# Optimization experiments

Hardware: AMD Instinct MI355X
Metric: run time of the kernel (lower is better)

## Reference

```python
import jax, jax.numpy as jnp
import numpy as np

N = 50000
E = 1600000
F_IN = 4
F_OUT = 32
PERIODS = 12


def setup_inputs() -> dict:
    key = jax.random.key(0)
    ks = jax.random.split(key, 18)
    s_in = 1.0 / np.sqrt(F_IN)
    s_cat = 1.0 / np.sqrt(2 * F_OUT)
    s_out = 1.0 / np.sqrt(F_OUT)
    inp = {
        'x': jax.random.normal(ks[0], (N, F_IN, PERIODS), dtype=jnp.float32),
        'edge_index': jax.random.randint(ks[1], (2, E), 0, N, dtype=jnp.int32),
        'attention': jax.random.uniform(ks[2], (PERIODS,), dtype=jnp.float32),
        # GRU update gate z: GCNConv weight/bias + Linear(2*F_OUT -> F_OUT)
        'Wz': jax.random.normal(ks[3], (F_IN, F_OUT), jnp.float32) * s_in,
        'bz': jnp.zeros((F_OUT,), jnp.float32),
        'Lz': jax.random.normal(ks[4], (2 * F_OUT, F_OUT), jnp.float32) * s_cat,
        'lz': jnp.zeros((F_OUT,), jnp.float32),
        # reset gate r
        'Wr': jax.random.normal(ks[5], (F_IN, F_OUT), jnp.float32) * s_in,
        'br': jnp.zeros((F_OUT,), jnp.float32),
        'Lr': jax.random.normal(ks[6], (2 * F_OUT, F_OUT), jnp.float32) * s_cat,
        'lr': jnp.zeros((F_OUT,), jnp.float32),
        # candidate h
        'Wh': jax.random.normal(ks[7], (F_IN, F_OUT), jnp.float32) * s_in,
        'bh': jnp.zeros((F_OUT,), jnp.float32),
        'Lh': jax.random.normal(ks[8], (2 * F_OUT, F_OUT), jnp.float32) * s_cat,
        'lh': jnp.zeros((F_OUT,), jnp.float32),
        # outer Linear(32 -> periods)
        'Wo': jax.random.normal(ks[9], (F_OUT, PERIODS), jnp.float32) * s_out,
        'bo': jnp.zeros((PERIODS,), jnp.float32),
    }
    return inp


def reference(x, edge_index, attention, Wz, bz, Lz, lz, Wr, br, Lr, lr, Wh, bh, Lh, lh, Wo, bo):
    n = x.shape[0]
    # gcn_norm: add self loops, symmetric D^-1/2 (A+I) D^-1/2
    loop = jnp.arange(n, dtype=edge_index.dtype)
    row = jnp.concatenate([edge_index[0], loop])  # source
    col = jnp.concatenate([edge_index[1], loop])  # target
    w = jnp.ones(row.shape[0], dtype=x.dtype)
    deg = jax.ops.segment_sum(w, col, num_segments=n)
    dinv = jnp.where(deg > 0, jax.lax.rsqrt(deg), 0.0)
    norm = dinv[row] * dinv[col]  # [E+N]

    def conv(xt, W, b):
        h = xt @ W                                   # [N, F_OUT]
        msg = h[row] * norm[:, None]                 # gather + scale
        return jax.ops.segment_sum(msg, col, num_segments=n) + b

    H0 = jnp.zeros((n, F_OUT), dtype=x.dtype)  # A3TGCN passes H=None each period

    def tgcn(xt):
        Z = jax.nn.sigmoid(jnp.concatenate([conv(xt, Wz, bz), H0], axis=1) @ Lz + lz)
        R = jax.nn.sigmoid(jnp.concatenate([conv(xt, Wr, br), H0], axis=1) @ Lr + lr)
        Ht = jnp.tanh(jnp.concatenate([conv(xt, Wh, bh), H0 * R], axis=1) @ Lh + lh)
        return Z * H0 + (1.0 - Z) * Ht

    Hs = jax.vmap(tgcn)(jnp.moveaxis(x, 2, 0))       # [T, N, F_OUT]
    probs = jax.nn.softmax(attention)
    H = jnp.einsum('tnc,t->nc', Hs, probs)           # attention-weighted sum over periods
    return jax.nn.relu(H) @ Wo + bo                  # [N, PERIODS]
```

## Files before the change

kernel.cpp:

```cpp
#include <hip/hip_runtime.h>
#include <hip/hip_fp16.h>
#include <math.h>

#define CHUNK 6144
#define CAPG  10240
#define GNODES 42

union U4H { uint4 u; __half2 h[4]; };

__global__ void k_pre(const float* __restrict__ Wz, const float* __restrict__ Lz, const float* __restrict__ lz,
                      const float* __restrict__ Wh, const float* __restrict__ Lh, const float* __restrict__ lh,
                      const float* __restrict__ bz, const float* __restrict__ bh,
                      const float* __restrict__ att,
                      float* __restrict__ AzT, float* __restrict__ AhT,
                      float* __restrict__ bzp, float* __restrict__ bhp, float* __restrict__ probs,
                      int* __restrict__ gcur) {
  int t = threadIdx.x;
  gcur[t] = 0;
  if (t < 128) {
    int f = t >> 2, k = t & 3;
    float s = 0.f, s2 = 0.f;
    for (int j = 0; j < 32; ++j) {
      s  = fmaf(Wz[k * 32 + j], Lz[j * 32 + f], s);
      s2 = fmaf(Wh[k * 32 + j], Lh[j * 32 + f], s2);
    }
    AzT[t] = s; AhT[t] = s2;
  }
  if (t >= 128 && t < 160) {
    int f = t - 128;
    float s = lz[f], s2 = lh[f];
    for (int j = 0; j < 32; ++j) {
      s  = fmaf(bz[j], Lz[j * 32 + f], s);
      s2 = fmaf(bh[j], Lh[j * 32 + f], s2);
    }
    bzp[f] = s; bhp[f] = s2;
  }
  if (t == 160) {
    float m = att[0];
    for (int i = 1; i < 12; ++i) m = fmaxf(m, att[i]);
    float e[12]; float s = 0.f;
    for (int i = 0; i < 12; ++i) { e[i] = __expf(att[i] - m); s += e[i]; }
    for (int i = 0; i < 12; ++i) probs[i] = e[i] / s;
  }
}

__global__ __launch_bounds__(1024) void k_part(const int* __restrict__ row, const int* __restrict__ col,
                                               int E, int nbkt,
                                               int* __restrict__ gcur, unsigned* __restrict__ part) {
  __shared__ unsigned spak[CHUNK];
  __shared__ unsigned char sbkt[CHUNK];
  __shared__ unsigned char slc[CHUNK];
  __shared__ int hist[256], sscan[256], scur[256], gbase[256];
  int t = threadIdx.x;
  int base = blockIdx.x * CHUNK;
  int cnt = E - base; if (cnt > CHUNK) cnt = CHUNK;
  if (t < 256) hist[t] = 0;
  __syncthreads();
  for (int i = t; i < cnt; i += 1024) {
    int c = col[base + i];
    int b = c >> 8;
    sbkt[i] = (unsigned char)b;
    slc[i]  = (unsigned char)(c & 255);
    atomicAdd(&hist[b], 1);
  }
  __syncthreads();
  int v = 0;
  if (t < 256) { v = hist[t]; sscan[t] = v; }
  __syncthreads();
  for (int off = 1; off < 256; off <<= 1) {
    int a = 0;
    if (t < 256 && t >= off) a = sscan[t - off];
    __syncthreads();
    if (t < 256) sscan[t] += a;
    __syncthreads();
  }
  if (t < 256) {
    sscan[t] -= v;
    gbase[t] = (v > 0) ? atomicAdd(&gcur[t], v) : 0;
    scur[t] = 0;
  }
  __syncthreads();
  for (int i = t; i < cnt; i += 1024) {
    int r = row[base + i];
    int b = sbkt[i];
    int pos = atomicAdd(&scur[b], 1);
    spak[sscan[b] + pos] = ((unsigned)r << 8) | (unsigned)slc[i];
  }
  __syncthreads();
  int wave = t >> 6, lane = t & 63;
  for (int b = wave; b < nbkt; b += 16) {
    int len = hist[b], gb = gbase[b], src = sscan[b];
    int lim = CAPG - gb; if (lim > len) lim = len;
    unsigned* dst = part + (size_t)b * CAPG + gb;
    for (int j = lane; j < lim; j += 64) dst[j] = spak[src + j];
  }
}

__global__ __launch_bounds__(1024) void k_sort(const unsigned* __restrict__ part, const int* __restrict__ gcur,
                                               const float4* __restrict__ x4,
                                               int* __restrict__ csr, int2* __restrict__ rng,
                                               float* __restrict__ dinv, uint2* __restrict__ xh2, int n) {
  __shared__ int hist[256], soff[256], scur2[256];
  __shared__ float sdi[256];
  int b = blockIdx.x, t = threadIdx.x;
  int cnt = gcur[b]; if (cnt > CAPG) cnt = CAPG;
  const unsigned* src = part + (size_t)b * CAPG;
  if (t < 256) hist[t] = 0;
  __syncthreads();
  for (int i = t; i < cnt; i += 1024) atomicAdd(&hist[src[i] & 255u], 1);
  __syncthreads();
  int v = 0;
  if (t < 256) { v = hist[t]; soff[t] = v; }
  __syncthreads();
  for (int off = 1; off < 256; off <<= 1) {
    int a = 0;
    if (t < 256 && t >= off) a = soff[t - off];
    __syncthreads();
    if (t < 256) soff[t] += a;
    __syncthreads();
  }
  int base = b * CAPG;
  if (t < 256) {
    int excl = soff[t] - v;
    int node = b * 256 + t;
    float di = rsqrtf((float)(v + 1));
    sdi[t] = di;
    if (node < n) {
      rng[node] = make_int2(base + excl, base + excl + v);
      dinv[node] = di;
    }
    soff[t] = excl;
    scur2[t] = 0;
  }
  __syncthreads();
  for (int i = t; i < cnt; i += 1024) {
    unsigned e = src[i];
    int lc = (int)(e & 255u);
    int pos = atomicAdd(&scur2[lc], 1);
    csr[base + soff[lc] + pos] = (int)(e >> 8);
  }
  int gb = b * 3072;
  for (int j = t; j < 3072; j += 1024) {
    int gi = gb + j;
    if (gi < n * 12) {
      float4 f = x4[gi];
      float d = sdi[j / 12];
      __half2 h0 = __floats2half2_rn(d * f.x, d * f.y);
      __half2 h1 = __floats2half2_rn(d * f.z, d * f.w);
      uint2 u; u.x = *(unsigned*)&h0; u.y = *(unsigned*)&h1;
      xh2[gi] = u;
    }
  }
}

__global__ __launch_bounds__(256) void k_gather(const int* __restrict__ csr, const int2* __restrict__ rng,
                                                const float* __restrict__ dinv, const uint4* __restrict__ xh4,
                                                const float* __restrict__ AzT, const float* __restrict__ AhT,
                                                const float* __restrict__ bzp, const float* __restrict__ bhp,
                                                const float* __restrict__ probs,
                                                const float* __restrict__ Wo, const float* __restrict__ bo,
                                                float* __restrict__ out, int n) {
  __shared__ float sY[GNODES * 49];
  __shared__ float4 sAz4[32], sAh4[32];
  __shared__ float sbzp[32], sbhp[32], sprobs[12], sbo[12], sWo[384];
  int t = threadIdx.x;
  int nb = blockIdx.x * GNODES;

  if (t < 32) {
    sAz4[t] = ((const float4*)AzT)[t];
    sAh4[t] = ((const float4*)AhT)[t];
    sbzp[t] = bzp[t]; sbhp[t] = bhp[t];
  }
  if (t >= 32 && t < 44) { sprobs[t - 32] = probs[t - 32]; sbo[t - 32] = bo[t - 32]; }
  for (int i = t; i < 384; i += 256) sWo[i] = Wo[i];

  int grp = t / 6, c = t - grp * 6;
  int node = nb + grp;
  if (t < GNODES * 6 && node < n) {
    U4H u; u.u = xh4[(size_t)node * 6 + c];
    float2 f0 = __half22float2(u.h[0]), f1 = __half22float2(u.h[1]);
    float2 f2 = __half22float2(u.h[2]), f3 = __half22float2(u.h[3]);
    float a0 = f0.x, a1 = f0.y, a2 = f1.x, a3 = f1.y;
    float a4 = f2.x, a5 = f2.y, a6 = f3.x, a7 = f3.y;
    int2 r = rng[node];
    int e = r.x, end = r.y;
    for (; e + 4 <= end; e += 4) {
      int r0 = csr[e], r1 = csr[e + 1], r2 = csr[e + 2], r3 = csr[e + 3];
      U4H v0, v1, v2, v3;
      v0.u = xh4[(size_t)r0 * 6 + c];
      v1.u = xh4[(size_t)r1 * 6 + c];
      v2.u = xh4[(size_t)r2 * 6 + c];
      v3.u = xh4[(size_t)r3 * 6 + c];
#define ACC8(V) { \
      float2 g0 = __half22float2(V.h[0]), g1 = __half22float2(V.h[1]); \
      float2 g2 = __half22float2(V.h[2]), g3 = __half22float2(V.h[3]); \
      a0 += g0.x; a1 += g0.y; a2 += g1.x; a3 += g1.y; \
      a4 += g2.x; a5 += g2.y; a6 += g3.x; a7 += g3.y; }
      ACC8(v0) ACC8(v1) ACC8(v2) ACC8(v3)
    }
    for (; e < end; ++e) {
      int r0 = csr[e];
      U4H v0; v0.u = xh4[(size_t)r0 * 6 + c];
      ACC8(v0)
    }
#undef ACC8
    float di = dinv[node];
    float* yb = sY + grp * 49 + c * 8;
    yb[0] = a0 * di; yb[1] = a1 * di; yb[2] = a2 * di; yb[3] = a3 * di;
    yb[4] = a4 * di; yb[5] = a5 * di; yb[6] = a6 * di; yb[7] = a7 * di;
  }
  __syncthreads();

  if (t < GNODES) {
    int node2 = nb + t;
    if (node2 < n) {
      const float* y = sY + t * 49;
      float H[32];
      for (int f = 0; f < 32; ++f) {
        float4 az = sAz4[f], ah = sAh4[f];
        float bzf = sbzp[f], bhf = sbhp[f];
        float acc = 0.f;
#pragma unroll
        for (int tt = 0; tt < 12; ++tt) {
          float y0 = y[tt], y1 = y[12 + tt], y2 = y[24 + tt], y3 = y[36 + tt];
          float za = fmaf(az.x, y0, fmaf(az.y, y1, fmaf(az.z, y2, fmaf(az.w, y3, bzf))));
          float ha = fmaf(ah.x, y0, fmaf(ah.y, y1, fmaf(ah.z, y2, fmaf(ah.w, y3, bhf))));
          float ez = __expf(za);
          float ax = fabsf(ha);
          float e2 = __expf(-2.f * ax);
          float g = (1.f - e2) / ((1.f + ez) * (1.f + e2));
          acc = fmaf(sprobs[tt], copysignf(g, ha), acc);
        }
        H[f] = fmaxf(acc, 0.f);
      }
#pragma unroll
      for (int p = 0; p < 12; ++p) {
        float acc = sbo[p];
#pragma unroll
        for (int f = 0; f < 32; ++f) acc = fmaf(H[f], sWo[f * 12 + p], acc);
        out[node2 * 12 + p] = acc;
      }
    }
  }
}

extern "C" void kernel_launch(void* const* d_in, const int* in_sizes, int n_in,
                              void* d_out, int out_size, void* d_ws, size_t ws_size,
                              hipStream_t stream) {
  const float* x   = (const float*)d_in[0];
  const int*   ei  = (const int*)d_in[1];
  const float* att = (const float*)d_in[2];
  const float* Wz  = (const float*)d_in[3];
  const float* bz  = (const float*)d_in[4];
  const float* Lz  = (const float*)d_in[5];
  const float* lz  = (const float*)d_in[6];
  const float* Wh  = (const float*)d_in[11];
  const float* bh  = (const float*)d_in[12];
  const float* Lh  = (const float*)d_in[13];
  const float* lh  = (const float*)d_in[14];
  const float* Wo  = (const float*)d_in[15];
  const float* bo  = (const float*)d_in[16];
  float* out = (float*)d_out;

  const int N = in_sizes[0] / (4 * 12);
  const int E = in_sizes[1] / 2;
  const int NBKT = (N + 255) >> 8;
  const int* row = ei;
  const int* col = ei + E;

  char* w = (char*)d_ws;
  size_t o = 0;
  auto alloc = [&](size_t bytes) -> char* {
    o = (o + 255) & ~(size_t)255;
    char* p = w + o; o += bytes; return p;
  };
  float* pAzT   = (float*)alloc(128 * 4);
  float* pAhT   = (float*)alloc(128 * 4);
  float* pbzp   = (float*)alloc(32 * 4);
  float* pbhp   = (float*)alloc(32 * 4);
  float* pprobs = (float*)alloc(12 * 4);
  int*   pgcur  = (int*)alloc(256 * 4);
  float* pdinv  = (float*)alloc((size_t)NBKT * 256 * 4);
  int2*  prng   = (int2*)alloc((size_t)N * 8);
  unsigned* ppart = (unsigned*)alloc((size_t)256 * CAPG * 4);
  int*   pcsr   = (int*)alloc((size_t)256 * CAPG * 4);
  uint2* pxh    = (uint2*)alloc((size_t)NBKT * 256 * 12 * 8);
  (void)ws_size; (void)n_in; (void)out_size;

  k_pre<<<1, 256, 0, stream>>>(Wz, Lz, lz, Wh, Lh, lh, bz, bh, att,
                               pAzT, pAhT, pbzp, pbhp, pprobs, pgcur);
  k_part<<<(E + CHUNK - 1) / CHUNK, 1024, 0, stream>>>(row, col, E, NBKT, pgcur, ppart);
  k_sort<<<NBKT, 1024, 0, stream>>>(ppart, pgcur, (const float4*)x, pcsr, prng, pdinv, pxh, N);
  k_gather<<<(N + GNODES - 1) / GNODES, 256, 0, stream>>>(pcsr, prng, pdinv, (const uint4*)pxh,
                                                          pAzT, pAhT, pbzp, pbhp, pprobs,
                                                          Wo, bo, out, N);
}
```

Measured before the change: 207.6 us.

## Split gather and dense stages into separate kernels with finer thread mapping

```diff
diff --git a/kernel.cpp b/kernel.cpp
--- a/kernel.cpp
+++ b/kernel.cpp
@@ -4,9 +4,9 @@
 
 #define CHUNK 6144
 #define CAPG  10240
-#define GNODES 42
-
-union U4H { uint4 u; __half2 h[4]; };
+#define GNODES 21
+
+union U2H { uint2 u; __half2 h[2]; };
 
 __global__ void k_pre(const float* __restrict__ Wz, const float* __restrict__ Lz, const float* __restrict__ lz,
                       const float* __restrict__ Wh, const float* __restrict__ Lh, const float* __restrict__ lh,
@@ -154,92 +154,104 @@
 }
 
 __global__ __launch_bounds__(256) void k_gather(const int* __restrict__ csr, const int2* __restrict__ rng,
-                                                const float* __restrict__ dinv, const uint4* __restrict__ xh4,
-                                                const float* __restrict__ AzT, const float* __restrict__ AhT,
-                                                const float* __restrict__ bzp, const float* __restrict__ bhp,
-                                                const float* __restrict__ probs,
-                                                const float* __restrict__ Wo, const float* __restrict__ bo,
-                                                float* __restrict__ out, int n) {
-  __shared__ float sY[GNODES * 49];
+                                                const float* __restrict__ dinv, const uint2* __restrict__ xh2,
+                                                float4* __restrict__ Y4, int n) {
+  int t = threadIdx.x;
+  int grp = t / 12, c = t - grp * 12;
+  if (grp >= GNODES) return;
+  int node = blockIdx.x * GNODES + grp;
+  if (node >= n) return;
+  U2H s; s.u = xh2[(size_t)node * 12 + c];
+  float2 f0 = __half22float2(s.h[0]), f1 = __half22float2(s.h[1]);
+  float a0 = f0.x, a1 = f0.y, a2 = f1.x, a3 = f1.y;
+  int2 r = rng[node];
+  int e = r.x, end = r.y;
+#define ACC4(V) { \
+    float2 g0 = __half22float2(V.h[0]), g1 = __half22float2(V.h[1]); \
+    a0 += g0.x; a1 += g0.y; a2 += g1.x; a3 += g1.y; }
+  for (; e + 8 <= end; e += 8) {
+    int r0 = csr[e],     r1 = csr[e + 1], r2 = csr[e + 2], r3 = csr[e + 3];
+    int r4 = csr[e + 4], r5 = csr[e + 5], r6 = csr[e + 6], r7 = csr[e + 7];
+    U2H v0, v1, v2, v3, v4, v5, v6, v7;
+    v0.u = xh2[(size_t)r0 * 12 + c];
+    v1.u = xh2[(size_t)r1 * 12 + c];
+    v2.u = xh2[(size_t)r2 * 12 + c];
+    v3.u = xh2[(size_t)r3 * 12 + c];
+    v4.u = xh2[(size_t)r4 * 12 + c];
+    v5.u = xh2[(size_t)r5 * 12 + c];
+    v6.u = xh2[(size_t)r6 * 12 + c];
+    v7.u = xh2[(size_t)r7 * 12 + c];
+    ACC4(v0) ACC4(v1) ACC4(v2) ACC4(v3) ACC4(v4) ACC4(v5) ACC4(v6) ACC4(v7)
+  }
+  for (; e < end; ++e) {
+    int r0 = csr[e];
+    U2H v0; v0.u = xh2[(size_t)r0 * 12 + c];
+    ACC4(v0)
+  }
+#undef ACC4
+  float di = dinv[node];
+  Y4[(size_t)node * 12 + c] = make_float4(a0 * di, a1 * di, a2 * di, a3 * di);
+}
+
+__global__ __launch_bounds__(256) void k_dense(
+    const float4* __restrict__ Y4,
+    const float* __restrict__ AzT, const float* __restrict__ AhT,
+    const float* __restrict__ bzp, const float* __restrict__ bhp,
+    const float* __restrict__ probs,
+    const float* __restrict__ Wo, const float* __restrict__ bo,
+    float* __restrict__ out, int n) {
   __shared__ float4 sAz4[32], sAh4[32];
-  __shared__ float sbzp[32], sbhp[32], sprobs[12], sbo[12], sWo[384];
+  __shared__ float sbzp[32], sbhp[32], sprobs[12], sbo[12];
+  __shared__ float sWo[384];
+  __shared__ float4 sY4[96];
+  __shared__ float sH[8 * 33];
+
   int t = threadIdx.x;
-  int nb = blockIdx.x * GNODES;
+  int nb = blockIdx.x * 8;
 
   if (t < 32) {
     sAz4[t] = ((const float4*)AzT)[t];
     sAh4[t] = ((const float4*)AhT)[t];
-    sbzp[t] = bzp[t]; sbhp[t] = bhp[t];
+    sbzp[t] = bzp[t];
+    sbhp[t] = bhp[t];
   }
   if (t >= 32 && t < 44) { sprobs[t - 32] = probs[t - 32]; sbo[t - 32] = bo[t - 32]; }
   for (int i = t; i < 384; i += 256) sWo[i] = Wo[i];
-
-  int grp = t / 6, c = t - grp * 6;
-  int node = nb + grp;
-  if (t < GNODES * 6 && node < n) {
-    U4H u; u.u = xh4[(size_t)node * 6 + c];
-    float2 f0 = __half22float2(u.h[0]), f1 = __half22float2(u.h[1]);
-    float2 f2 = __half22float2(u.h[2]), f3 = __half22float2(u.h[3]);
-    float a0 = f0.x, a1 = f0.y, a2 = f1.x, a3 = f1.y;
-    float a4 = f2.x, a5 = f2.y, a6 = f3.x, a7 = f3.y;
-    int2 r = rng[node];
-    int e = r.x, end = r.y;
-    for (; e + 4 <= end; e += 4) {
-      int r0 = csr[e], r1 = csr[e + 1], r2 = csr[e + 2], r3 = csr[e + 3];
-      U4H v0, v1, v2, v3;
-      v0.u = xh4[(size_t)r0 * 6 + c];
-      v1.u = xh4[(size_t)r1 * 6 + c];
-      v2.u = xh4[(size_t)r2 * 6 + c];
-      v3.u = xh4[(size_t)r3 * 6 + c];
-#define ACC8(V) { \
-      float2 g0 = __half22float2(V.h[0]), g1 = __half22float2(V.h[1]); \
-      float2 g2 = __half22float2(V.h[2]), g3 = __half22float2(V.h[3]); \
-      a0 += g0.x; a1 += g0.y; a2 += g1.x; a3 += g1.y; \
-      a4 += g2.x; a5 += g2.y; a6 += g3.x; a7 += g3.y; }
-      ACC8(v0) ACC8(v1) ACC8(v2) ACC8(v3)
-    }
-    for (; e < end; ++e) {
-      int r0 = csr[e];
-      U4H v0; v0.u = xh4[(size_t)r0 * 6 + c];
-      ACC8(v0)
-    }
-#undef ACC8
-    float di = dinv[node];
-    float* yb = sY + grp * 49 + c * 8;
-    yb[0] = a0 * di; yb[1] = a1 * di; yb[2] = a2 * di; yb[3] = a3 * di;
-    yb[4] = a4 * di; yb[5] = a5 * di; yb[6] = a6 * di; yb[7] = a7 * di;
-  }
-  __syncthreads();
-
-  if (t < GNODES) {
-    int node2 = nb + t;
+  if (t < 96) {
+    int gi = nb * 12 + t;
+    if (gi < n * 12) sY4[t] = Y4[gi];
+  }
+  __syncthreads();
+
+  int ln = t >> 5, f = t & 31;
+  float4 az = sAz4[f], ah = sAh4[f];
+  float bzf = sbzp[f], bhf = sbhp[f];
+  const float* y = (const float*)sY4 + ln * 48;
+  float Hf = 0.f;
+#pragma unroll
+  for (int tt = 0; tt < 12; ++tt) {
+    float y0 = y[tt], y1 = y[12 + tt], y2 = y[24 + tt], y3 = y[36 + tt];
+    float za = fmaf(az.x, y0, fmaf(az.y, y1, fmaf(az.z, y2, fmaf(az.w, y3, bzf))));
+    float ha = fmaf(ah.x, y0, fmaf(ah.y, y1, fmaf(ah.z, y2, fmaf(ah.w, y3, bhf))));
+    float ez = __expf(za);
+    float ax = fabsf(ha);
+    float e2 = __expf(-2.f * ax);
+    float g = (1.f - e2) / ((1.f + ez) * (1.f + e2));
+    Hf = fmaf(sprobs[tt], copysignf(g, ha), Hf);
+  }
+  sH[ln * 33 + f] = fmaxf(Hf, 0.f);
+  __syncthreads();
+
+  if (t < 96) {
+    int ln2 = t / 12, p = t - ln2 * 12;
+    int node2 = nb + ln2;
     if (node2 < n) {
-      const float* y = sY + t * 49;
-      float H[32];
-      for (int f = 0; f < 32; ++f) {
-        float4 az = sAz4[f], ah = sAh4[f];
-        float bzf = sbzp[f], bhf = sbhp[f];
-        float acc = 0.f;
+      float acc = sbo[p];
+      const float* h = &sH[ln2 * 33];
+      const float* wv = &sWo[p];
 #pragma unroll
-        for (int tt = 0; tt < 12; ++tt) {
-          float y0 = y[tt], y1 = y[12 + tt], y2 = y[24 + tt], y3 = y[36 + tt];
-          float za = fmaf(az.x, y0, fmaf(az.y, y1, fmaf(az.z, y2, fmaf(az.w, y3, bzf))));
-          float ha = fmaf(ah.x, y0, fmaf(ah.y, y1, fmaf(ah.z, y2, fmaf(ah.w, y3, bhf))));
-          float ez = __expf(za);
-          float ax = fabsf(ha);
-          float e2 = __expf(-2.f * ax);
-          float g = (1.f - e2) / ((1.f + ez) * (1.f + e2));
-          acc = fmaf(sprobs[tt], copysignf(g, ha), acc);
-        }
-        H[f] = fmaxf(acc, 0.f);
-      }
-#pragma unroll
-      for (int p = 0; p < 12; ++p) {
-        float acc = sbo[p];
-#pragma unroll
-        for (int f = 0; f < 32; ++f) acc = fmaf(H[f], sWo[f * 12 + p], acc);
-        out[node2 * 12 + p] = acc;
-      }
+      for (int f2 = 0; f2 < 32; ++f2) acc = fmaf(h[f2], wv[f2 * 12], acc);
+      out[node2 * 12 + p] = acc;
     }
   }
 }
@@ -285,13 +297,15 @@
   unsigned* ppart = (unsigned*)alloc((size_t)256 * CAPG * 4);
   int*   pcsr   = (int*)alloc((size_t)256 * CAPG * 4);
   uint2* pxh    = (uint2*)alloc((size_t)NBKT * 256 * 12 * 8);
+  float* pY     = (float*)alloc((size_t)N * 48 * 4);
   (void)ws_size; (void)n_in; (void)out_size;
 
   k_pre<<<1, 256, 0, stream>>>(Wz, Lz, lz, Wh, Lh, lh, bz, bh, att,
                                pAzT, pAhT, pbzp, pbhp, pprobs, pgcur);
   k_part<<<(E + CHUNK - 1) / CHUNK, 1024, 0, stream>>>(row, col, E, NBKT, pgcur, ppart);
   k_sort<<<NBKT, 1024, 0, stream>>>(ppart, pgcur, (const float4*)x, pcsr, prng, pdinv, pxh, N);
-  k_gather<<<(N + GNODES - 1) / GNODES, 256, 0, stream>>>(pcsr, prng, pdinv, (const uint4*)pxh,
-                                                          pAzT, pAhT, pbzp, pbhp, pprobs,
-                                                          Wo, bo, out, N);
-}
+  k_gather<<<(N + GNODES - 1) / GNODES, 256, 0, stream>>>(pcsr, prng, pdinv, pxh,
+                                                          (float4*)pY, N);
+  k_dense<<<(N + 7) / 8, 256, 0, stream>>>((const float4*)pY, pAzT, pAhT, pbzp, pbhp, pprobs,
+                                           Wo, bo, out, N);
+}
```

New measurement: 179.8 us. 13.4% less time.
